# Optimization experiments

Hardware: AMD Instinct MI355X
Metric: run time of the kernel (lower is better)

Reference implementation:

```python
import jax, jax.numpy as jnp
import numpy as np

N_HEAD = 16

def _phi(x):
    # silu(x) + 1 feature map
    return jax.nn.silu(x) + 1.0

def setup_inputs() -> dict:
    key = jax.random.key(0)
    ks = jax.random.split(key, 8)
    B, T, D = 8, 4096, 1024
    s = 0.02
    return {
        "x":  jax.random.normal(ks[0], (B, T, D), jnp.float32),
        "Wq": jax.random.normal(ks[1], (D, D), jnp.float32) * s,
        "bq": jax.random.normal(ks[2], (D,), jnp.float32) * s,
        "Wk": jax.random.normal(ks[3], (D, D), jnp.float32) * s,
        "Wv": jax.random.normal(ks[4], (D, D), jnp.float32) * s,
        "bv": jax.random.normal(ks[5], (D,), jnp.float32) * s,
        "Wo": jax.random.normal(ks[6], (D, D), jnp.float32) * s,
        "bo": jax.random.normal(ks[7], (D,), jnp.float32) * s,
    }

def reference(x, Wq, bq, Wk, Wv, bv, Wo, bo):
    B, T, D = x.shape
    H = N_HEAD
    Dh = D // H
    scale = Dh ** (-0.25)
    # projections (torch F.linear: x @ W.T + b); key has no bias
    q = x @ Wq.T + bq
    k = x @ Wk.T
    v = x @ Wv.T + bv
    # [B, T, H, Dh] -> [B, H, T, Dh]
    q = q.reshape(B, T, H, Dh).transpose(0, 2, 1, 3) * scale
    k = k.reshape(B, T, H, Dh).transpose(0, 2, 1, 3) * scale
    v = v.reshape(B, T, H, Dh).transpose(0, 2, 1, 3)
    phi_q = _phi(q)
    phi_k = _phi(k)
    # kv: [B, H, Dh, Dh] = sum_t phi_k[t]^T v[t]
    kv = jnp.einsum('bhtd,bhte->bhde', phi_k, v)
    out = jnp.einsum('bhtd,bhde->bhte', phi_q, kv)  # [B, H, T, Dh]
    wv = out.transpose(0, 2, 1, 3).reshape(B, T, D)
    return wv @ Wo.T + bo
```

## Files before the change

kernel.cpp:

```cpp
#include <hip/hip_runtime.h>
#include <math.h>

typedef short bf16x8 __attribute__((ext_vector_type(8)));
typedef float f32x4  __attribute__((ext_vector_type(4)));

__device__ __forceinline__ float phi_act(float t) {
    return t / (1.0f + __expf(-t)) + 1.0f;
}

__device__ __forceinline__ unsigned short f2bf(float f) {
    union { float f; unsigned int u; } un; un.f = f;
    unsigned int r = un.u + 0x7fffu + ((un.u >> 16) & 1u);
    return (unsigned short)(r >> 16);
}

__device__ __forceinline__ void gload_lds16(const void* g, void* l) {
    __builtin_amdgcn_global_load_lds(
        (const __attribute__((address_space(1))) void*)g,
        (__attribute__((address_space(3))) void*)l, 16, 0, 0);
}

__device__ __forceinline__ void gemm_body_mfma(
    const unsigned short* __restrict__ A, const unsigned short* __restrict__ W,
    const float* __restrict__ bias, float* __restrict__ outF,
    unsigned short* __restrict__ outB,
    int N, int K, int mode, float scale)
{
    __shared__ unsigned short As[128 * 32];
    __shared__ unsigned short Bs[128 * 32];

    const int tid  = threadIdx.x;
    const int lane = tid & 63;
    const int w    = tid >> 6;
    const int wm   = w >> 1, wn = w & 1;
    const int bm   = blockIdx.y, bn = blockIdx.x;

    const int lrow = lane >> 2;
    const int kcol = (lane & 3) * 8;
    const int c0   = w * 2;

    const size_t arow0 = (size_t)(bm * 128);
    const size_t brow0 = (size_t)(bn * 128);

    f32x4 zero4 = {0.f, 0.f, 0.f, 0.f};
    f32x4 acc[4][4];
    #pragma unroll
    for (int i = 0; i < 4; i++)
        #pragma unroll
        for (int j = 0; j < 4; j++) acc[i][j] = zero4;

    const int kq = lane >> 4;
    const int ml = lane & 15;

    for (int k0 = 0; k0 < K; k0 += 32) {
        __syncthreads();
        #pragma unroll
        for (int u = 0; u < 2; u++) {
            const int c = c0 + u;
            const int row = c * 16 + lrow;
            gload_lds16(A + (arow0 + row) * K + k0 + kcol, &As[c * 512]);
            gload_lds16(W + (brow0 + row) * K + k0 + kcol, &Bs[c * 512]);
        }
        __syncthreads();

        bf16x8 af[4], bfr[4];
        #pragma unroll
        for (int mi = 0; mi < 4; mi++)
            af[mi] = *(const bf16x8*)&As[(wm * 64 + mi * 16 + ml) * 32 + kq * 8];
        #pragma unroll
        for (int nj = 0; nj < 4; nj++)
            bfr[nj] = *(const bf16x8*)&Bs[(wn * 64 + nj * 16 + ml) * 32 + kq * 8];

        #pragma unroll
        for (int mi = 0; mi < 4; mi++)
            #pragma unroll
            for (int nj = 0; nj < 4; nj++)
                acc[mi][nj] = __builtin_amdgcn_mfma_f32_16x16x32_bf16(
                    af[mi], bfr[nj], acc[mi][nj], 0, 0, 0);
    }

    const int rq = lane >> 4;
    const int cl = lane & 15;
    #pragma unroll
    for (int nj = 0; nj < 4; nj++) {
        const int col = bn * 128 + wn * 64 + nj * 16 + cl;
        const float bvv = bias ? bias[col] : 0.f;
        #pragma unroll
        for (int mi = 0; mi < 4; mi++) {
            const int rowb = bm * 128 + wm * 64 + mi * 16 + rq * 4;
            #pragma unroll
            for (int r = 0; r < 4; r++) {
                float v = acc[mi][nj][r] + bvv;
                const size_t idx = (size_t)(rowb + r) * N + col;
                if (mode == 0) {
                    outF[idx] = v;
                } else {
                    if (mode == 1) v = phi_act(v * scale);
                    outB[idx] = f2bf(v);
                }
            }
        }
    }
}

__global__ __launch_bounds__(256) void qkv_gemm_mfma(
    const unsigned short* __restrict__ xb,
    const unsigned short* __restrict__ wqb, const float* __restrict__ bq,
    const unsigned short* __restrict__ wkb,
    const unsigned short* __restrict__ wvb, const float* __restrict__ bv,
    unsigned short* __restrict__ phiq, unsigned short* __restrict__ phik,
    unsigned short* __restrict__ vb,
    int N, int K, float scale)
{
    const int z = blockIdx.z;
    if (z == 0)      gemm_body_mfma(xb, wqb, bq,      nullptr, phiq, N, K, 1, scale);
    else if (z == 1) gemm_body_mfma(xb, wkb, nullptr, nullptr, phik, N, K, 1, scale);
    else             gemm_body_mfma(xb, wvb, bv,      nullptr, vb,   N, K, 2, 1.0f);
}

__global__ __launch_bounds__(256) void out_gemm_mfma(
    const unsigned short* __restrict__ A, const unsigned short* __restrict__ W,
    const float* __restrict__ bias, float* __restrict__ C, int N, int K)
{
    gemm_body_mfma(A, W, bias, C, nullptr, N, K, 0, 1.0f);
}

__global__ __launch_bounds__(256) void cast_all(
    const float* __restrict__ x,  unsigned short* __restrict__ xb,
    const float* __restrict__ w0, unsigned short* __restrict__ w0b,
    const float* __restrict__ w1, unsigned short* __restrict__ w1b,
    const float* __restrict__ w2, unsigned short* __restrict__ w2b,
    const float* __restrict__ w3, unsigned short* __restrict__ w3b,
    size_t nx, size_t nw)
{
    size_t i = ((size_t)blockIdx.x * 256 + threadIdx.x) * 4;
    const float* s; unsigned short* d; size_t off;
    if (i < nx)               { s = x;  d = xb;  off = i; }
    else if (i < nx + nw)     { s = w0; d = w0b; off = i - nx; }
    else if (i < nx + 2 * nw) { s = w1; d = w1b; off = i - nx - nw; }
    else if (i < nx + 3 * nw) { s = w2; d = w2b; off = i - nx - 2 * nw; }
    else                      { s = w3; d = w3b; off = i - nx - 3 * nw; }
    float4 v = *(const float4*)(s + off);
    ushort4 o;
    o.x = f2bf(v.x); o.y = f2bf(v.y); o.z = f2bf(v.z); o.w = f2bf(v.w);
    *(ushort4*)(d + off) = o;
}

__global__ __launch_bounds__(256) void kv_part(
    const unsigned short* __restrict__ phiK, const unsigned short* __restrict__ V,
    float* __restrict__ partial, int Ttot, int D)
{
    const int tc = blockIdx.x, bh = blockIdx.y;
    const int b = bh >> 4, h = bh & 15;
    const int tbase = tc * 512;

    __shared__ unsigned short pkT[64][72];
    __shared__ unsigned short vvT[64][72];

    const int tid  = threadIdx.x;
    const int lane = tid & 63;
    const int w    = tid >> 6;
    const int dq = w >> 1, eq = w & 1;
    const int kq = lane >> 4, ml = lane & 15;

    f32x4 zero4 = {0.f, 0.f, 0.f, 0.f};
    f32x4 acc[2][2];
    acc[0][0] = zero4; acc[0][1] = zero4; acc[1][0] = zero4; acc[1][1] = zero4;

    const size_t base = (size_t)b * Ttot * D + h * 64;

    for (int c8 = 0; c8 < 8; c8++) {
        const int t0 = tbase + c8 * 64;
        __syncthreads();
        #pragma unroll
        for (int u = 0; u < 2; u++) {
            const int f = tid * 2 + u;
            const int trow = f >> 3;
            const int d8 = (f & 7) * 8;
            const size_t g = base + (size_t)(t0 + trow) * D + d8;
            uint4 kk = *(const uint4*)(phiK + g);
            uint4 vv = *(const uint4*)(V + g);
            pkT[d8 + 0][trow] = (unsigned short)(kk.x & 0xffff);
            pkT[d8 + 1][trow] = (unsigned short)(kk.x >> 16);
            pkT[d8 + 2][trow] = (unsigned short)(kk.y & 0xffff);
            pkT[d8 + 3][trow] = (unsigned short)(kk.y >> 16);
            pkT[d8 + 4][trow] = (unsigned short)(kk.z & 0xffff);
            pkT[d8 + 5][trow] = (unsigned short)(kk.z >> 16);
            pkT[d8 + 6][trow] = (unsigned short)(kk.w & 0xffff);
            pkT[d8 + 7][trow] = (unsigned short)(kk.w >> 16);
            vvT[d8 + 0][trow] = (unsigned short)(vv.x & 0xffff);
            vvT[d8 + 1][trow] = (unsigned short)(vv.x >> 16);
            vvT[d8 + 2][trow] = (unsigned short)(vv.y & 0xffff);
            vvT[d8 + 3][trow] = (unsigned short)(vv.y >> 16);
            vvT[d8 + 4][trow] = (unsigned short)(vv.z & 0xffff);
            vvT[d8 + 5][trow] = (unsigned short)(vv.z >> 16);
            vvT[d8 + 6][trow] = (unsigned short)(vv.w & 0xffff);
            vvT[d8 + 7][trow] = (unsigned short)(vv.w >> 16);
        }
        __syncthreads();

        #pragma unroll
        for (int ks = 0; ks < 2; ks++) {
            bf16x8 af[2], bfv[2];
            #pragma unroll
            for (int ai = 0; ai < 2; ai++)
                af[ai] = *(const bf16x8*)&pkT[dq * 32 + ai * 16 + ml][ks * 32 + kq * 8];
            #pragma unroll
            for (int bi = 0; bi < 2; bi++)
                bfv[bi] = *(const bf16x8*)&vvT[eq * 32 + bi * 16 + ml][ks * 32 + kq * 8];
            #pragma unroll
            for (int ai = 0; ai < 2; ai++)
                #pragma unroll
                for (int bi = 0; bi < 2; bi++)
                    acc[ai][bi] = __builtin_amdgcn_mfma_f32_16x16x32_bf16(
                        af[ai], bfv[bi], acc[ai][bi], 0, 0, 0);
        }
    }

    float* outp = partial + ((size_t)bh * 8 + tc) * 4096;
    const int rq = lane >> 4, cl = lane & 15;
    #pragma unroll
    for (int ai = 0; ai < 2; ai++)
        #pragma unroll
        for (int bi = 0; bi < 2; bi++) {
            const int e = eq * 32 + bi * 16 + cl;
            #pragma unroll
            for (int r = 0; r < 4; r++) {
                const int d = dq * 32 + ai * 16 + rq * 4 + r;
                outp[d * 64 + e] = acc[ai][bi][r];
            }
        }
}

__global__ __launch_bounds__(256) void kv_reduce(
    const float* __restrict__ partial, unsigned short* __restrict__ kvT)
{
    const int bh = blockIdx.x;
    const int tid = threadIdx.x;
    __shared__ float s[64][65];
    float a[16];
    #pragma unroll
    for (int c = 0; c < 16; c++) a[c] = 0.f;
    #pragma unroll
    for (int p = 0; p < 8; p++) {
        const float* src = partial + ((size_t)bh * 8 + p) * 4096;
        #pragma unroll
        for (int c = 0; c < 16; c++) a[c] += src[c * 256 + tid];
    }
    #pragma unroll
    for (int c = 0; c < 16; c++) {
        const int idx = c * 256 + tid;
        s[idx >> 6][idx & 63] = a[c];
    }
    __syncthreads();
    unsigned short* outp = kvT + (size_t)bh * 4096;
    #pragma unroll
    for (int c = 0; c < 16; c++) {
        const int j = c * 256 + tid;
        outp[j] = f2bf(s[j & 63][j >> 6]);
    }
}

__global__ __launch_bounds__(256) void av_mfma(
    const unsigned short* __restrict__ phiQ, const unsigned short* __restrict__ kvT,
    unsigned short* __restrict__ Oattn, int Ttot, int D)
{
    const int bh = blockIdx.y;
    const int b = bh >> 4, h = bh & 15;
    const int t0 = blockIdx.x * 256;

    __shared__ unsigned short Aq[256 * 64];
    __shared__ unsigned short Kv[64][72];

    const int tid  = threadIdx.x;
    const int lane = tid & 63;
    const int w    = tid >> 6;
    const int kq = lane >> 4, ml = lane & 15;

    {
        const int e = tid >> 2;
        const int c16 = (tid & 3) * 16;
        const unsigned short* src = kvT + (size_t)bh * 4096 + e * 64 + c16;
        *(uint4*)&Kv[e][c16]     = *(const uint4*)(src);
        *(uint4*)&Kv[e][c16 + 8] = *(const uint4*)(src + 8);
    }
    {
        const int lr = lane >> 3;
        const int d8 = (lane & 7) * 8;
        #pragma unroll
        for (int r = 0; r < 8; r++) {
            const int chunk = r * 4 + w;
            const int row = chunk * 8 + lr;
            gload_lds16(phiQ + ((size_t)(b * Ttot + t0 + row)) * D + h * 64 + d8,
                        &Aq[chunk * 512]);
        }
    }
    __syncthreads();

    f32x4 zero4 = {0.f, 0.f, 0.f, 0.f};
    f32x4 acc[4][4];
    #pragma unroll
    for (int i = 0; i < 4; i++)
        #pragma unroll
        for (int j = 0; j < 4; j++) acc[i][j] = zero4;

    #pragma unroll
    for (int ks = 0; ks < 2; ks++) {
        bf16x8 af[4], bfv[4];
        #pragma unroll
        for (int mi = 0; mi < 4; mi++)
            af[mi] = *(const bf16x8*)&Aq[(w * 64 + mi * 16 + ml) * 64 + ks * 32 + kq * 8];
        #pragma unroll
        for (int nj = 0; nj < 4; nj++)
            bfv[nj] = *(const bf16x8*)&Kv[nj * 16 + ml][ks * 32 + kq * 8];
        #pragma unroll
        for (int mi = 0; mi < 4; mi++)
            #pragma unroll
            for (int nj = 0; nj < 4; nj++)
                acc[mi][nj] = __builtin_amdgcn_mfma_f32_16x16x32_bf16(
                    af[mi], bfv[nj], acc[mi][nj], 0, 0, 0);
    }

    const int rq = lane >> 4, cl = lane & 15;
    #pragma unroll
    for (int mi = 0; mi < 4; mi++) {
        #pragma unroll
        for (int r = 0; r < 4; r++) {
            const int t = t0 + w * 64 + mi * 16 + rq * 4 + r;
            unsigned short* dst = Oattn + (size_t)(b * Ttot + t) * D + h * 64;
            #pragma unroll
            for (int nj = 0; nj < 4; nj++)
                dst[nj * 16 + cl] = f2bf(acc[mi][nj][r]);
        }
    }
}

extern "C" void kernel_launch(void* const* d_in, const int* in_sizes, int n_in,
                              void* d_out, int out_size, void* d_ws, size_t ws_size,
                              hipStream_t stream) {
    const float* x  = (const float*)d_in[0];
    const float* Wq = (const float*)d_in[1];
    const float* bq = (const float*)d_in[2];
    const float* Wk = (const float*)d_in[3];
    const float* Wv = (const float*)d_in[4];
    const float* bv = (const float*)d_in[5];
    const float* Wo = (const float*)d_in[6];
    const float* bo = (const float*)d_in[7];
    float* out = (float*)d_out;

    const int B = 8, T = 4096, D = 1024;
    const int M = B * T;
    const float scale = 0.35355339059327379f;
    const size_t MD = (size_t)M * D;
    const size_t WN = (size_t)D * D;

    unsigned short* xb    = (unsigned short*)d_ws;
    unsigned short* wqb   = xb + MD;
    unsigned short* wkb   = wqb + WN;
    unsigned short* wvb   = wkb + WN;
    unsigned short* wob   = wvb + WN;
    unsigned short* phiq  = wob + WN;
    unsigned short* phik  = phiq + MD;
    unsigned short* vb    = phik + MD;
    unsigned short* oat   = vb + MD;
    float*          part  = (float*)(oat + MD);
    unsigned short* kvT   = (unsigned short*)(part + (size_t)1024 * 4096);
    (void)ws_size; (void)in_sizes; (void)n_in; (void)out_size;

    dim3 blk(256);

    {
        size_t total4 = (MD + 4 * WN) / 4;
        cast_all<<<dim3((unsigned)(total4 / 256)), blk, 0, stream>>>(
            x, xb, Wq, wqb, Wk, wkb, Wv, wvb, Wo, wob, MD, WN);
    }

    qkv_gemm_mfma<<<dim3(D / 128, M / 128, 3), blk, 0, stream>>>(
        xb, wqb, bq, wkb, wvb, bv, phiq, phik, vb, D, D, scale);

    kv_part<<<dim3(8, 128), blk, 0, stream>>>(phik, vb, part, T, D);
    kv_reduce<<<dim3(128), blk, 0, stream>>>(part, kvT);

    av_mfma<<<dim3(T / 256, 128), blk, 0, stream>>>(phiq, kvT, oat, T, D);

    out_gemm_mfma<<<dim3(D / 128, M / 128), blk, 0, stream>>>(oat, wob, bo, out, D, D);
}
```

Baseline: 717.0 us.

## Replace GEMMs with 256x256 double-buffered swizzled MFMA kernel and XCD block remap

```diff
diff --git a/kernel.cpp b/kernel.cpp
--- a/kernel.cpp
+++ b/kernel.cpp
@@ -20,109 +20,184 @@
         (__attribute__((address_space(3))) void*)l, 16, 0, 0);
 }
 
-__device__ __forceinline__ void gemm_body_mfma(
+
+__device__ __forceinline__ void stage_half(const unsigned short* __restrict__ g,
+                                           unsigned short* l, int tid) {
+    const int wb = tid & ~63;
+    #pragma unroll
+    for (int u = 0; u < 2; u++) {
+        const int p  = (u * 512 + tid) * 16;
+        const int qq = p ^ (((p >> 7) & 7) << 4);
+        gload_lds16((const char*)g + (size_t)(qq >> 7) * 2048 + (qq & 127),
+                    (char*)l + (size_t)(u * 512 + wb) * 16);
+    }
+}
+
+#define LOAD_AF(buf, ah) do {                                                   \
+    const char* _s = (const char*)&As[buf][ah][0];                              \
+    _Pragma("unroll")                                                           \
+    for (int _mi = 0; _mi < 4; _mi++) {                                         \
+        const int _row = qm * 64 + _mi * 16 + ml;                               \
+        const int _sw = (_row & 7) << 4;                                        \
+        _Pragma("unroll")                                                       \
+        for (int _ks = 0; _ks < 2; _ks++)                                       \
+            af[_mi][_ks] = *(const bf16x8*)(_s +                                \
+                (((_row * 128) + _ks * 64 + kq * 16) ^ _sw));                   \
+    }                                                                           \
+} while (0)
+
+#define LOAD_BF(buf, bh) do {                                                   \
+    const char* _s = (const char*)&Bs[buf][bh][0];                              \
+    _Pragma("unroll")                                                           \
+    for (int _nj = 0; _nj < 2; _nj++) {                                         \
+        const int _col = qn * 32 + _nj * 16 + ml;                               \
+        const int _sw = (_col & 7) << 4;                                        \
+        _Pragma("unroll")                                                       \
+        for (int _ks = 0; _ks < 2; _ks++)                                       \
+            bf[_nj][_ks] = *(const bf16x8*)(_s +                                \
+                (((_col * 128) + _ks * 64 + kq * 16) ^ _sw));                   \
+    }                                                                           \
+} while (0)
+
+#define PHASE_MFMA(Q) do {                                                      \
+    __builtin_amdgcn_s_barrier();                                               \
+    asm volatile("s_waitcnt lgkmcnt(0)" ::: "memory");                          \
+    __builtin_amdgcn_sched_barrier(0);                                          \
+    __builtin_amdgcn_s_setprio(1);                                              \
+    _Pragma("unroll")                                                           \
+    for (int _mi = 0; _mi < 4; _mi++)                                           \
+        _Pragma("unroll")                                                       \
+        for (int _nj = 0; _nj < 2; _nj++)                                       \
+            _Pragma("unroll")                                                   \
+            for (int _ks = 0; _ks < 2; _ks++)                                   \
+                acc[Q][_mi][_nj] = __builtin_amdgcn_mfma_f32_16x16x32_bf16(     \
+                    af[_mi][_ks], bf[_nj][_ks], acc[Q][_mi][_nj], 0, 0, 0);     \
+    __builtin_amdgcn_s_setprio(0);                                              \
+    __builtin_amdgcn_s_barrier();                                               \
+} while (0)
+
+template<int KIND>
+__device__ __forceinline__ void gemm256_body(
     const unsigned short* __restrict__ A, const unsigned short* __restrict__ W,
-    const float* __restrict__ bias, float* __restrict__ outF,
-    unsigned short* __restrict__ outB,
-    int N, int K, int mode, float scale)
-{
-    __shared__ unsigned short As[128 * 32];
-    __shared__ unsigned short Bs[128 * 32];
+    const float* __restrict__ bq, const float* __restrict__ bv,
+    unsigned short* __restrict__ oq, unsigned short* __restrict__ okk,
+    unsigned short* __restrict__ ov, float* __restrict__ outF,
+    const float* __restrict__ bo, float scale, int NBN)
+{
+    __shared__ __align__(128) unsigned short As[2][2][128 * 64];
+    __shared__ __align__(128) unsigned short Bs[2][2][128 * 64];
 
     const int tid  = threadIdx.x;
     const int lane = tid & 63;
     const int w    = tid >> 6;
-    const int wm   = w >> 1, wn = w & 1;
-    const int bm   = blockIdx.y, bn = blockIdx.x;
-
-    const int lrow = lane >> 2;
-    const int kcol = (lane & 3) * 8;
-    const int c0   = w * 2;
-
-    const size_t arow0 = (size_t)(bm * 128);
-    const size_t brow0 = (size_t)(bn * 128);
-
+    const int qm   = w >> 2;
+    const int qn   = w & 3;
+    const int ml   = lane & 15;
+    const int kq   = lane >> 4;
+
+    const int nwg  = (int)gridDim.x;
+    const int bid  = (int)blockIdx.x;
+    const int sbid = (bid & 7) * (nwg >> 3) + (bid >> 3);
+    const int bn   = sbid % NBN;
+    const int bm   = sbid / NBN;
+
+    const unsigned short* Ab = A + (size_t)bm * 256 * 1024;
+    const unsigned short* Bb = W + (size_t)bn * 256 * 1024;
+
+    f32x4 acc[4][4][2];
     f32x4 zero4 = {0.f, 0.f, 0.f, 0.f};
-    f32x4 acc[4][4];
-    #pragma unroll
-    for (int i = 0; i < 4; i++)
-        #pragma unroll
-        for (int j = 0; j < 4; j++) acc[i][j] = zero4;
-
-    const int kq = lane >> 4;
-    const int ml = lane & 15;
-
-    for (int k0 = 0; k0 < K; k0 += 32) {
-        __syncthreads();
-        #pragma unroll
-        for (int u = 0; u < 2; u++) {
-            const int c = c0 + u;
-            const int row = c * 16 + lrow;
-            gload_lds16(A + (arow0 + row) * K + k0 + kcol, &As[c * 512]);
-            gload_lds16(W + (brow0 + row) * K + k0 + kcol, &Bs[c * 512]);
-        }
-        __syncthreads();
-
-        bf16x8 af[4], bfr[4];
+    #pragma unroll
+    for (int q = 0; q < 4; q++)
         #pragma unroll
         for (int mi = 0; mi < 4; mi++)
-            af[mi] = *(const bf16x8*)&As[(wm * 64 + mi * 16 + ml) * 32 + kq * 8];
-        #pragma unroll
-        for (int nj = 0; nj < 4; nj++)
-            bfr[nj] = *(const bf16x8*)&Bs[(wn * 64 + nj * 16 + ml) * 32 + kq * 8];
-
-        #pragma unroll
-        for (int mi = 0; mi < 4; mi++)
-            #pragma unroll
-            for (int nj = 0; nj < 4; nj++)
-                acc[mi][nj] = __builtin_amdgcn_mfma_f32_16x16x32_bf16(
-                    af[mi], bfr[nj], acc[mi][nj], 0, 0, 0);
-    }
-
-    const int rq = lane >> 4;
-    const int cl = lane & 15;
-    #pragma unroll
-    for (int nj = 0; nj < 4; nj++) {
-        const int col = bn * 128 + wn * 64 + nj * 16 + cl;
-        const float bvv = bias ? bias[col] : 0.f;
-        #pragma unroll
-        for (int mi = 0; mi < 4; mi++) {
-            const int rowb = bm * 128 + wm * 64 + mi * 16 + rq * 4;
-            #pragma unroll
-            for (int r = 0; r < 4; r++) {
-                float v = acc[mi][nj][r] + bvv;
-                const size_t idx = (size_t)(rowb + r) * N + col;
-                if (mode == 0) {
-                    outF[idx] = v;
-                } else {
-                    if (mode == 1) v = phi_act(v * scale);
-                    outB[idx] = f2bf(v);
+            #pragma unroll
+            for (int nj = 0; nj < 2; nj++) acc[q][mi][nj] = zero4;
+
+    bf16x8 af[4][2], bf[2][2];
+
+    stage_half(Ab,                   &As[0][0][0], tid);
+    stage_half(Bb + 128 * 1024,      &Bs[0][1][0], tid);
+    stage_half(Ab + 128 * 1024,      &As[0][1][0], tid);
+    stage_half(Bb,                   &Bs[0][0][0], tid);
+    stage_half(Ab + 64,              &As[1][0][0], tid);
+    stage_half(Bb + 128 * 1024 + 64, &Bs[1][1][0], tid);
+
+    for (int t = 0; t < 16; ++t) {
+        const int buf = t & 1;
+        if (t == 15) { asm volatile("s_waitcnt vmcnt(0)" ::: "memory"); }
+        else         { asm volatile("s_waitcnt vmcnt(4)" ::: "memory"); }
+        __builtin_amdgcn_s_barrier();
+
+        LOAD_AF(buf, 0);
+        LOAD_BF(buf, 0);
+        if (t + 1 < 16) stage_half(Ab + 128 * 1024 + (t + 1) * 64, &As[buf ^ 1][1][0], tid);
+        PHASE_MFMA(0);
+
+        LOAD_BF(buf, 1);
+        if (t + 1 < 16) stage_half(Bb + (t + 1) * 64, &Bs[buf ^ 1][0][0], tid);
+        PHASE_MFMA(1);
+
+        LOAD_AF(buf, 1);
+        if (t + 2 < 16) stage_half(Ab + (t + 2) * 64, &As[buf][0][0], tid);
+        PHASE_MFMA(2);
+
+        LOAD_BF(buf, 0);
+        if (t + 2 < 16) stage_half(Bb + 128 * 1024 + (t + 2) * 64, &Bs[buf][1][0], tid);
+        PHASE_MFMA(3);
+    }
+
+    const int rq = lane >> 4, cl = lane & 15;
+    #pragma unroll
+    for (int q = 0; q < 4; q++) {
+        const int qr = (q >> 1) * 128;
+        const int qc = ((q == 1) || (q == 2)) ? 128 : 0;
+        #pragma unroll
+        for (int nj = 0; nj < 2; nj++) {
+            const int colg = bn * 256 + qc + qn * 32 + nj * 16 + cl;
+            if constexpr (KIND == 0) {
+                const int z    = colg >> 10;
+                const int lcol = colg & 1023;
+                const float bias = (z == 0) ? bq[lcol] : ((z == 2) ? bv[lcol] : 0.f);
+                unsigned short* dst = (z == 0) ? oq : ((z == 1) ? okk : ov);
+                #pragma unroll
+                for (int mi = 0; mi < 4; mi++) {
+                    const int row0 = bm * 256 + qr + qm * 64 + mi * 16 + rq * 4;
+                    #pragma unroll
+                    for (int r = 0; r < 4; r++) {
+                        float vv = acc[q][mi][nj][r] + bias;
+                        if (z < 2) vv = phi_act(vv * scale);
+                        dst[(size_t)(row0 + r) * 1024 + lcol] = f2bf(vv);
+                    }
+                }
+            } else {
+                const float bias = bo[colg];
+                #pragma unroll
+                for (int mi = 0; mi < 4; mi++) {
+                    const int row0 = bm * 256 + qr + qm * 64 + mi * 16 + rq * 4;
+                    #pragma unroll
+                    for (int r = 0; r < 4; r++)
+                        outF[(size_t)(row0 + r) * 1024 + colg] = acc[q][mi][nj][r] + bias;
                 }
             }
         }
     }
 }
 
-__global__ __launch_bounds__(256) void qkv_gemm_mfma(
+__global__ __launch_bounds__(512, 2) void qkv_gemm256(
     const unsigned short* __restrict__ xb,
-    const unsigned short* __restrict__ wqb, const float* __restrict__ bq,
-    const unsigned short* __restrict__ wkb,
-    const unsigned short* __restrict__ wvb, const float* __restrict__ bv,
+    const unsigned short* __restrict__ wcat,
+    const float* __restrict__ bq, const float* __restrict__ bv,
     unsigned short* __restrict__ phiq, unsigned short* __restrict__ phik,
-    unsigned short* __restrict__ vb,
-    int N, int K, float scale)
-{
-    const int z = blockIdx.z;
-    if (z == 0)      gemm_body_mfma(xb, wqb, bq,      nullptr, phiq, N, K, 1, scale);
-    else if (z == 1) gemm_body_mfma(xb, wkb, nullptr, nullptr, phik, N, K, 1, scale);
-    else             gemm_body_mfma(xb, wvb, bv,      nullptr, vb,   N, K, 2, 1.0f);
-}
-
-__global__ __launch_bounds__(256) void out_gemm_mfma(
+    unsigned short* __restrict__ vb, float scale)
+{
+    gemm256_body<0>(xb, wcat, bq, bv, phiq, phik, vb, nullptr, nullptr, scale, 12);
+}
+
+__global__ __launch_bounds__(512, 2) void out_gemm256(
     const unsigned short* __restrict__ A, const unsigned short* __restrict__ W,
-    const float* __restrict__ bias, float* __restrict__ C, int N, int K)
-{
-    gemm_body_mfma(A, W, bias, C, nullptr, N, K, 0, 1.0f);
+    const float* __restrict__ bo, float* __restrict__ out)
+{
+    gemm256_body<1>(A, W, nullptr, nullptr, nullptr, nullptr, nullptr, out, bo, 1.0f, 4);
 }
 
 __global__ __launch_bounds__(256) void cast_all(
@@ -375,13 +450,13 @@
             x, xb, Wq, wqb, Wk, wkb, Wv, wvb, Wo, wob, MD, WN);
     }
 
-    qkv_gemm_mfma<<<dim3(D / 128, M / 128, 3), blk, 0, stream>>>(
-        xb, wqb, bq, wkb, wvb, bv, phiq, phik, vb, D, D, scale);
+    qkv_gemm256<<<dim3(1536), dim3(512), 0, stream>>>(
+        xb, wqb, bq, bv, phiq, phik, vb, scale);
 
     kv_part<<<dim3(8, 128), blk, 0, stream>>>(phik, vb, part, T, D);
     kv_reduce<<<dim3(128), blk, 0, stream>>>(part, kvT);
 
     av_mfma<<<dim3(T / 256, 128), blk, 0, stream>>>(phiq, kvT, oat, T, D);
 
-    out_gemm_mfma<<<dim3(D / 128, M / 128), blk, 0, stream>>>(oat, wob, bo, out, D, D);
-}
+    out_gemm256<<<dim3(512), dim3(512), 0, stream>>>(oat, wob, bo, out);
+}
```

Result: faster. 668.7 us (-6.7%).
